# Optimization experiments

Hardware: AMD Instinct MI355X
Metric: run time of the kernel (lower is better)

## Reference

```python
import jax, jax.numpy as jnp
import numpy as np

EPS = 1e-5

def _bn(x, g, b, m, v):
    return (x - m) * jax.lax.rsqrt(v + EPS) * g + b

def setup_inputs() -> dict:
    key = jax.random.key(0)
    ks = jax.random.split(key, 40)
    B, D, H, O = 4096, 1723 * 6, 1024, 24 * 9 + 10
    d = {"x": jax.random.normal(ks[0], (B, D), jnp.float32)}
    def lin(i, din, dout):
        return (jax.random.normal(ks[i], (din, dout), jnp.float32) * (1.0 / np.sqrt(din)),
                jax.random.normal(ks[i + 1], (dout,), jnp.float32) * 0.01)
    def bnp(i, dout):
        return (jax.random.normal(ks[i], (dout,), jnp.float32) * 0.1 + 1.0,
                jax.random.normal(ks[i + 1], (dout,), jnp.float32) * 0.1,
                jax.random.normal(ks[i + 2], (dout,), jnp.float32) * 0.1,
                jax.random.uniform(ks[i + 3], (dout,), jnp.float32, 0.5, 1.5))
    d["W1"], d["b1"] = lin(1, D, H); d["g1"], d["be1"], d["m1"], d["v1"] = bnp(3, H)
    d["Wa"], d["ba"] = lin(7, H, H); d["ga"], d["bea"], d["ma"], d["va"] = bnp(9, H)
    d["Wb"], d["bb"] = lin(13, H, H); d["gb"], d["beb"], d["mb"], d["vb"] = bnp(15, H)
    d["Wc"], d["bc"] = lin(19, H, H); d["gc"], d["bec"], d["mc"], d["vc"] = bnp(21, H)
    d["Wd"], d["bd"] = lin(25, H, H); d["gd"], d["bed"], d["md"], d["vd"] = bnp(27, H)
    d["Wf"], d["bf"] = lin(31, H, O)
    return d

def reference(x, W1, b1, g1, be1, m1, v1,
              Wa, ba, ga, bea, ma, va,
              Wb, bb, gb, beb, mb, vb,
              Wc, bc, gc, bec, mc, vc,
              Wd, bd, gd, bed, md, vd,
              Wf, bf):
    B = x.shape[0]
    # FCBlock: Linear -> BN -> ReLU
    h = jax.nn.relu(_bn(x @ W1 + b1, g1, be1, m1, v1))
    # FCResBlock 1: relu(h + BN(Linear(relu(BN(Linear(h))))))
    t = jax.nn.relu(_bn(h @ Wa + ba, ga, bea, ma, va))
    t = _bn(t @ Wb + bb, gb, beb, mb, vb)
    h = jax.nn.relu(h + t)
    # FCResBlock 2
    t = jax.nn.relu(_bn(h @ Wc + bc, gc, bec, mc, vc))
    t = _bn(t @ Wd + bd, gd, bed, md, vd)
    h = jax.nn.relu(h + t)
    out = h @ Wf + bf  # [B, 226]
    rot = out[:, :216].reshape(-1, 3, 3)  # [B*24, 3, 3]
    betas = out[:, 216:]                   # [B, 10]
    U, S, Vh = jnp.linalg.svd(rot)         # batched 3x3 SVD
    R = jnp.matmul(U, Vh)                  # U V^T, closest orthogonal matrix
    det = jax.lax.stop_gradient(jnp.linalg.det(R))[:, None, None]  # torch computes det under no_grad
    R = (R * det).reshape(B, 24, 3, 3)
    return (R, betas)
```

## Files before the change

### kernel.cpp

```cpp
#include <hip/hip_runtime.h>
#include <hip/hip_bf16.h>

typedef unsigned int u32;
typedef unsigned short u16;
typedef _Float16 f16;
typedef __attribute__((ext_vector_type(8))) f16 f16x8;
typedef __attribute__((ext_vector_type(4))) float f32x4;
typedef __attribute__((ext_vector_type(4))) u16 u16x4;

#define NB 4096
#define DIN 10338
#define DPAD 10368
#define KC 5184
#define HD 1024
#define OD 226
#define OPAD 256
#define BN_EPS 1e-5f
#define RSC 0.00048828125f

__device__ __forceinline__ u16 f2h(float v) {
  f16 h = (f16)v;
  u16 r;
  __builtin_memcpy(&r, &h, 2);
  return r;
}
__device__ __forceinline__ void split2(float a, u16& s0, u16& s1) {
  f16 h0 = (f16)a;
  float r = (a - (float)h0) * 2048.0f;
  __builtin_memcpy(&s0, &h0, 2);
  s1 = f2h(r);
}

__device__ __forceinline__ void gload_lds16(const u16* g, u16* l) {
  __builtin_amdgcn_global_load_lds(
      (const __attribute__((address_space(1))) u32*)g,
      (__attribute__((address_space(3))) u32*)l, 16, 0, 0);
}

__global__ __launch_bounds__(256) void k_split_x(const float* __restrict__ x,
                                                 f16* __restrict__ p0,
                                                 f16* __restrict__ p1) {
  u32 idx = (blockIdx.x * 256u + threadIdx.x) * 4u;
  u32 row = idx / DPAD;
  u32 col = idx - row * DPAD;
  const float* s = x + (size_t)row * DIN + col;
  float v[4];
#pragma unroll
  for (int i = 0; i < 4; i++) {
    v[i] = ((int)col + i < DIN) ? s[i] : 0.f;
  }
  u16x4 o0, o1;
#pragma unroll
  for (int i = 0; i < 4; i++) {
    u16 a0, a1;
    split2(v[i], a0, a1);
    o0[i] = a0;
    o1[i] = a1;
  }
  *(u16x4*)((u16*)p0 + idx) = o0;
  *(u16x4*)((u16*)p1 + idx) = o1;
}

__global__ __launch_bounds__(256) void k_split_w(const float* __restrict__ W,
                                                 f16* __restrict__ p0,
                                                 f16* __restrict__ p1, int K,
                                                 int N, int Kp) {
  __shared__ float tile[32][33];
  int k0 = blockIdx.x * 32, n0 = blockIdx.y * 32;
  int tx = threadIdx.x, ty = threadIdx.y;
#pragma unroll
  for (int i = 0; i < 4; i++) {
    int k = k0 + ty + i * 8, n = n0 + tx;
    tile[ty + i * 8][tx] = (k < K && n < N) ? W[(size_t)k * N + n] : 0.f;
  }
  __syncthreads();
#pragma unroll
  for (int i = 0; i < 4; i++) {
    int n = n0 + ty + i * 8, k = k0 + tx;
    u16 s0, s1;
    split2(tile[tx][ty + i * 8], s0, s1);
    size_t o = (size_t)n * Kp + k;
    ((u16*)p0)[o] = s0;
    ((u16*)p1)[o] = s1;
  }
}

__global__ __launch_bounds__(512, 2) void k_gemm_big(
    const f16* __restrict__ A0p, const f16* __restrict__ A1p,
    const f16* __restrict__ B0p, const f16* __restrict__ B1p,
    float* __restrict__ P, int ldA, int ldB, int nk) {
  __shared__ __align__(16) u16 lds[3 * 24576];

  const u32 gx = gridDim.x, gy = gridDim.y;
  const u32 nwg = gx * gy * gridDim.z;
  u32 lin = blockIdx.x + gx * (blockIdx.y + gy * blockIdx.z);
  {
    const u32 q = nwg >> 3, r = nwg & 7;
    const u32 xcd = lin & 7, o = lin >> 3;
    lin = (xcd < r ? xcd * (q + 1) : r * (q + 1) + (xcd - r) * q) + o;
  }
  const u32 bz = lin / (gx * gy);
  const u32 rem = lin - bz * gx * gy;
  const u32 by = rem / gx;
  const u32 bx = rem - by * gx;
  const int m0 = by * 256, n0 = bx * 128;
  const size_t kbase = (size_t)bz * KC;

  const u16* __restrict__ A0u = (const u16*)A0p + kbase;
  const u16* __restrict__ A1u = (const u16*)A1p + kbase;
  const u16* __restrict__ B0u = (const u16*)B0p + kbase;
  const u16* __restrict__ B1u = (const u16*)B1p + kbase;
  float* __restrict__ Pz = P + (size_t)bz * NB * HD;

  const int t = threadIdx.x;
  const int lane = t & 63;
  const int wid = t >> 6;
  const int wm = wid >> 1, wn = wid & 1;
  const int l15 = lane & 15, l4 = lane >> 4;

  const int sgc = (((t & 3) ^ ((t >> 3) & 3)) << 3);
  const size_t gA0 = (size_t)(m0 + (t >> 2)) * ldA + sgc;
  const size_t gA1 = gA0 + (size_t)128 * ldA;
  const size_t gB = (size_t)(n0 + (t >> 2)) * ldB + sgc;
  const int dA0 = t * 8, dB = t * 8;

  int offA[4], offB[4];
#pragma unroll
  for (int mi = 0; mi < 4; mi++) {
    int row = wm * 64 + mi * 16 + l15;
    offA[mi] = row * 32 + ((l4 ^ ((row >> 1) & 3)) << 3);
  }
#pragma unroll
  for (int ni = 0; ni < 4; ni++) {
    int row = wn * 64 + ni * 16 + l15;
    offB[ni] = row * 32 + ((l4 ^ ((row >> 1) & 3)) << 3);
  }

  f32x4 hi[4][4], lo[4][4];
#pragma unroll
  for (int i = 0; i < 4; i++)
#pragma unroll
    for (int j = 0; j < 4; j++) {
      f32x4 z = {0.f, 0.f, 0.f, 0.f};
      hi[i][j] = z;
      lo[i][j] = z;
    }

#define STAGE_A0(Sb, ko)                         \
  gload_lds16(A0u + gA0 + (ko), (Sb) + dA0);     \
  gload_lds16(A0u + gA1 + (ko), (Sb) + 4096 + dA0);
#define STAGE_A1(Sb, ko)                              \
  gload_lds16(A1u + gA0 + (ko), (Sb) + 8192 + dA0);   \
  gload_lds16(A1u + gA1 + (ko), (Sb) + 12288 + dA0);
#define STAGE_B(Sb, ko)                               \
  gload_lds16(B0u + gB + (ko), (Sb) + 16384 + dB);    \
  gload_lds16(B1u + gB + (ko), (Sb) + 20480 + dB);

#define MFMA16(dst, af, bf)                                              \
  _Pragma("unroll") for (int mi = 0; mi < 4; mi++)                       \
      _Pragma("unroll") for (int ni = 0; ni < 4; ni++)                   \
          dst[mi][ni] = __builtin_amdgcn_mfma_f32_16x16x32_f16(          \
              af[mi], bf[ni], dst[mi][ni], 0, 0, 0);

  {
    u16* Sb0 = lds;
    u16* Sb1 = lds + 24576;
    STAGE_A0(Sb0, 0) STAGE_A1(Sb0, 0) STAGE_B(Sb0, 0)
    STAGE_A0(Sb1, 32) STAGE_A1(Sb1, 32) STAGE_B(Sb1, 32)
  }
  asm volatile("s_waitcnt vmcnt(6)" ::: "memory");
  __builtin_amdgcn_s_barrier();
  __builtin_amdgcn_sched_barrier(0);

  for (int tau = 0; tau < nk - 2; ++tau) {
    const u16* Lb = lds + (tau % 3) * 24576;
    u16* Sb = lds + ((tau + 2) % 3) * 24576;
    const size_t ko = (size_t)(tau + 2) * 32;
    f16x8 a0[4], b0[4], xf[4];

#pragma unroll
    for (int mi = 0; mi < 4; mi++) a0[mi] = *(const f16x8*)(Lb + offA[mi]);
#pragma unroll
    for (int ni = 0; ni < 4; ni++)
      b0[ni] = *(const f16x8*)(Lb + 16384 + offB[ni]);
    STAGE_A0(Sb, ko)
    __builtin_amdgcn_s_barrier();
    asm volatile("s_waitcnt lgkmcnt(0)" ::: "memory");
    __builtin_amdgcn_sched_barrier(0);
    __builtin_amdgcn_s_setprio(1);
    MFMA16(hi, a0, b0)
    __builtin_amdgcn_s_setprio(0);
    __builtin_amdgcn_s_barrier();

#pragma unroll
    for (int ni = 0; ni < 4; ni++)
      xf[ni] = *(const f16x8*)(Lb + 20480 + offB[ni]);
    STAGE_A1(Sb, ko)
    __builtin_amdgcn_s_barrier();
    asm volatile("s_waitcnt lgkmcnt(0)" ::: "memory");
    __builtin_amdgcn_sched_barrier(0);
    __builtin_amdgcn_s_setprio(1);
    MFMA16(lo, a0, xf)
    __builtin_amdgcn_s_setprio(0);
    __builtin_amdgcn_s_barrier();

#pragma unroll
    for (int mi = 0; mi < 4; mi++)
      xf[mi] = *(const f16x8*)(Lb + 8192 + offA[mi]);
    STAGE_B(Sb, ko)
    asm volatile("s_waitcnt vmcnt(6)" ::: "memory");
    __builtin_amdgcn_s_barrier();
    asm volatile("s_waitcnt lgkmcnt(0)" ::: "memory");
    __builtin_amdgcn_sched_barrier(0);
    __builtin_amdgcn_s_setprio(1);
    MFMA16(lo, xf, b0)
    __builtin_amdgcn_s_setprio(0);
    __builtin_amdgcn_s_barrier();
  }
  asm volatile("s_waitcnt vmcnt(0)" ::: "memory");
  __builtin_amdgcn_s_barrier();
  __builtin_amdgcn_sched_barrier(0);
#pragma unroll 1
  for (int tau = nk - 2; tau < nk; ++tau) {
    const u16* Lb = lds + (tau % 3) * 24576;
    f16x8 a0[4], b0[4], xf[4];
#pragma unroll
    for (int mi = 0; mi < 4; mi++) a0[mi] = *(const f16x8*)(Lb + offA[mi]);
#pragma unroll
    for (int ni = 0; ni < 4; ni++)
      b0[ni] = *(const f16x8*)(Lb + 16384 + offB[ni]);
    MFMA16(hi, a0, b0)
#pragma unroll
    for (int ni = 0; ni < 4; ni++)
      xf[ni] = *(const f16x8*)(Lb + 20480 + offB[ni]);
    MFMA16(lo, a0, xf)
#pragma unroll
    for (int mi = 0; mi < 4; mi++)
      xf[mi] = *(const f16x8*)(Lb + 8192 + offA[mi]);
    MFMA16(lo, xf, b0)
  }
#undef STAGE_A0
#undef STAGE_A1
#undef STAGE_B
#undef MFMA16

  const int rowb = m0 + wm * 64 + l4 * 4;
  const int colb = n0 + wn * 64 + l15;
#pragma unroll
  for (int mi = 0; mi < 4; mi++) {
#pragma unroll
    for (int ni = 0; ni < 4; ni++) {
      const int col = colb + ni * 16;
#pragma unroll
      for (int r = 0; r < 4; r++) {
        const int row = rowb + mi * 16 + r;
        Pz[(size_t)row * HD + col] = hi[mi][ni][r] + lo[mi][ni][r] * RSC;
      }
    }
  }
}

__global__ __launch_bounds__(256) void k_epi1(
    const float* __restrict__ P0, const float* __restrict__ P1,
    const float* __restrict__ bias, const float* __restrict__ gam,
    const float* __restrict__ bet, const float* __restrict__ mu,
    const float* __restrict__ var, float* __restrict__ hF,
    f16* __restrict__ h0, f16* __restrict__ h1) {
  const u32 i4 = (blockIdx.x * 256u + threadIdx.x) * 4u;
  const u32 col0 = i4 & (HD - 1);
  f32x4 a = *(const f32x4*)(P0 + i4);
  f32x4 b = *(const f32x4*)(P1 + i4);
  f32x4 y;
  u16x4 o0, o1;
#pragma unroll
  for (int e = 0; e < 4; e++) {
    const u32 c = col0 + e;
    float sc = gam[c] * rsqrtf(var[c] + BN_EPS);
    float v = ((a[e] + b[e]) + bias[c] - mu[c]) * sc + bet[c];
    v = fmaxf(v, 0.f);
    y[e] = v;
    u16 s0, s1;
    split2(v, s0, s1);
    o0[e] = s0;
    o1[e] = s1;
  }
  *(f32x4*)(hF + i4) = y;
  *(u16x4*)((u16*)h0 + i4) = o0;
  *(u16x4*)((u16*)h1 + i4) = o1;
}

template <int EPI>
__global__ __launch_bounds__(512, 2) void k_gemm_f(
    const f16* __restrict__ A0p, const f16* __restrict__ A1p,
    const f16* __restrict__ B0p, const f16* __restrict__ B1p,
    const float* __restrict__ bias, const float* __restrict__ gam,
    const float* __restrict__ bet, const float* __restrict__ mu,
    const float* __restrict__ var, const float* __restrict__ resF,
    float* __restrict__ hFout, f16* __restrict__ pl0, f16* __restrict__ pl1,
    float* __restrict__ oF, int ldA, int ldB, int nk, int ldout) {
  __shared__ __align__(16) u16 lds[4 * 16384];

  const u32 gx = gridDim.x, gy = gridDim.y;
  const u32 nwg = gx * gy;
  u32 lin = blockIdx.x + gx * blockIdx.y;
  {
    const u32 q = nwg >> 3, r = nwg & 7;
    const u32 xcd = lin & 7, o = lin >> 3;
    lin = (xcd < r ? xcd * (q + 1) : r * (q + 1) + (xcd - r) * q) + o;
  }
  const u32 by = lin / gx;
  const u32 bx = lin - by * gx;
  const int m0 = by * 128, n0 = bx * 128;

  const u16* __restrict__ A0u = (const u16*)A0p;
  const u16* __restrict__ A1u = (const u16*)A1p;
  const u16* __restrict__ B0u = (const u16*)B0p;
  const u16* __restrict__ B1u = (const u16*)B1p;

  const int t = threadIdx.x;
  const int lane = t & 63;
  const int wid = t >> 6;
  const int wm = wid >> 1, wn = wid & 1;
  const int l15 = lane & 15, l4 = lane >> 4;

  const int srow = t >> 2, sj = t & 3;
  const int sgc = ((sj ^ ((srow >> 1) & 3)) << 3);
  const size_t gA = (size_t)(m0 + srow) * ldA + sgc;
  const size_t gB = (size_t)(n0 + srow) * ldB + sgc;
  const int d0 = t * 8;

  int offA[2], offB[4];
#pragma unroll
  for (int mi = 0; mi < 2; mi++) {
    int row = wm * 32 + mi * 16 + l15;
    offA[mi] = row * 32 + ((l4 ^ ((row >> 1) & 3)) << 3);
  }
#pragma unroll
  for (int ni = 0; ni < 4; ni++) {
    int row = wn * 64 + ni * 16 + l15;
    offB[ni] = row * 32 + ((l4 ^ ((row >> 1) & 3)) << 3);
  }

  f32x4 hi[2][4], lo[2][4];
#pragma unroll
  for (int i = 0; i < 2; i++)
#pragma unroll
    for (int j = 0; j < 4; j++) {
      f32x4 z = {0.f, 0.f, 0.f, 0.f};
      hi[i][j] = z;
      lo[i][j] = z;
    }

#define STG_A0(Sb, ko) gload_lds16(A0u + gA + (ko), (Sb) + d0);
#define STG_A1(Sb, ko) gload_lds16(A1u + gA + (ko), (Sb) + 4096 + d0);
#define STG_B(Sb, ko)                               \
  gload_lds16(B0u + gB + (ko), (Sb) + 8192 + d0);   \
  gload_lds16(B1u + gB + (ko), (Sb) + 12288 + d0);
#define MFMA8(dst, af, bf)                                               \
  _Pragma("unroll") for (int mi = 0; mi < 2; mi++)                       \
      _Pragma("unroll") for (int ni = 0; ni < 4; ni++)                   \
          dst[mi][ni] = __builtin_amdgcn_mfma_f32_16x16x32_f16(          \
              af[mi], bf[ni], dst[mi][ni], 0, 0, 0);

  {
    u16* S0 = lds;
    u16* S1 = lds + 16384;
    u16* S2 = lds + 32768;
    STG_A0(S0, 0) STG_A1(S0, 0) STG_B(S0, 0)
    STG_A0(S1, 32) STG_A1(S1, 32) STG_B(S1, 32)
    STG_A0(S2, 64) STG_A1(S2, 64) STG_B(S2, 64)
  }
  asm volatile("s_waitcnt vmcnt(8)" ::: "memory");
  __builtin_amdgcn_s_barrier();
  __builtin_amdgcn_sched_barrier(0);

  for (int tau = 0; tau < nk - 3; ++tau) {
    const u16* Lb = lds + (tau & 3) * 16384;
    u16* Sb = lds + ((tau + 3) & 3) * 16384;
    const size_t ko = (size_t)(tau + 3) * 32;
    f16x8 a0[2], b0[4], xf[4];

#pragma unroll
    for (int mi = 0; mi < 2; mi++) a0[mi] = *(const f16x8*)(Lb + offA[mi]);
#pragma unroll
    for (int ni = 0; ni < 4; ni++)
      b0[ni] = *(const f16x8*)(Lb + 8192 + offB[ni]);
    STG_A0(Sb, ko)
    __builtin_amdgcn_s_barrier();
    asm volatile("s_waitcnt lgkmcnt(0)" ::: "memory");
    __builtin_amdgcn_sched_barrier(0);
    __builtin_amdgcn_s_setprio(1);
    MFMA8(hi, a0, b0)
    __builtin_amdgcn_s_setprio(0);
    __builtin_amdgcn_s_barrier();

#pragma unroll
    for (int ni = 0; ni < 4; ni++)
      xf[ni] = *(const f16x8*)(Lb + 12288 + offB[ni]);
    STG_A1(Sb, ko)
    __builtin_amdgcn_s_barrier();
    asm volatile("s_waitcnt lgkmcnt(0)" ::: "memory");
    __builtin_amdgcn_sched_barrier(0);
    __builtin_amdgcn_s_setprio(1);
    MFMA8(lo, a0, xf)
    __builtin_amdgcn_s_setprio(0);
    __builtin_amdgcn_s_barrier();

#pragma unroll
    for (int mi = 0; mi < 2; mi++)
      xf[mi] = *(const f16x8*)(Lb + 4096 + offA[mi]);
    STG_B(Sb, ko)
    asm volatile("s_waitcnt vmcnt(8)" ::: "memory");
    __builtin_amdgcn_s_barrier();
    asm volatile("s_waitcnt lgkmcnt(0)" ::: "memory");
    __builtin_amdgcn_sched_barrier(0);
    __builtin_amdgcn_s_setprio(1);
    MFMA8(lo, xf, b0)
    __builtin_amdgcn_s_setprio(0);
    __builtin_amdgcn_s_barrier();
  }
  asm volatile("s_waitcnt vmcnt(0)" ::: "memory");
  __builtin_amdgcn_s_barrier();
  __builtin_amdgcn_sched_barrier(0);
#pragma unroll 1
  for (int tau = nk - 3; tau < nk; ++tau) {
    const u16* Lb = lds + (tau & 3) * 16384;
    f16x8 a0[2], b0[4], xf[4];
#pragma unroll
    for (int mi = 0; mi < 2; mi++) a0[mi] = *(const f16x8*)(Lb + offA[mi]);
#pragma unroll
    for (int ni = 0; ni < 4; ni++)
      b0[ni] = *(const f16x8*)(Lb + 8192 + offB[ni]);
    MFMA8(hi, a0, b0)
#pragma unroll
    for (int ni = 0; ni < 4; ni++)
      xf[ni] = *(const f16x8*)(Lb + 12288 + offB[ni]);
    MFMA8(lo, a0, xf)
#pragma unroll
    for (int mi = 0; mi < 2; mi++)
      xf[mi] = *(const f16x8*)(Lb + 4096 + offA[mi]);
    MFMA8(lo, xf, b0)
  }
#undef STG_A0
#undef STG_A1
#undef STG_B
#undef MFMA8

  const int rowb = m0 + wm * 32 + l4 * 4;
  const int colb = n0 + wn * 64 + l15;
#pragma unroll
  for (int ni = 0; ni < 4; ni++) {
    const int col = colb + ni * 16;
    float sc = 1.f, pb = 0.f;
    if (EPI == 4) {
      pb = (col < OD) ? bias[col] : 0.f;
    } else {
      sc = gam[col] * rsqrtf(var[col] + BN_EPS);
      pb = (bias[col] - mu[col]) * sc + bet[col];
    }
#pragma unroll
    for (int mi = 0; mi < 2; mi++) {
#pragma unroll
      for (int r = 0; r < 4; r++) {
        const int row = rowb + mi * 16 + r;
        float s = hi[mi][ni][r] + lo[mi][ni][r] * RSC;
        if (EPI == 4) {
          oF[(size_t)row * ldout + col] = s + pb;
          continue;
        }
        float v = s * sc + pb;
        if (EPI == 2 || EPI == 3) v += resF[(size_t)row * HD + col];
        v = fmaxf(v, 0.f);
        if (EPI == 2) hFout[(size_t)row * HD + col] = v;
        u16 s0, s1;
        split2(v, s0, s1);
        size_t o = (size_t)row * HD + col;
        ((u16*)pl0)[o] = s0;
        ((u16*)pl1)[o] = s1;
      }
    }
  }
}

__global__ __launch_bounds__(256) void k_polar(const float* __restrict__ oF,
                                               float* __restrict__ R) {
  int g = blockIdx.x * 256 + threadIdx.x;
  if (g >= NB * 24) return;
  int b = g / 24, j = g - b * 24;
  const float* p = oF + (size_t)b * OPAD + j * 9;
  float xv[9];
#pragma unroll
  for (int e = 0; e < 9; e++) xv[e] = p[e];
#pragma unroll 1
  for (int it = 0; it < 18; it++) {
    float c0 = xv[4] * xv[8] - xv[5] * xv[7];
    float c1 = xv[5] * xv[6] - xv[3] * xv[8];
    float c2 = xv[3] * xv[7] - xv[4] * xv[6];
    float c3 = xv[2] * xv[7] - xv[1] * xv[8];
    float c4 = xv[0] * xv[8] - xv[2] * xv[6];
    float c5 = xv[1] * xv[6] - xv[0] * xv[7];
    float c6 = xv[1] * xv[5] - xv[2] * xv[4];
    float c7 = xv[2] * xv[3] - xv[0] * xv[5];
    float c8 = xv[0] * xv[4] - xv[1] * xv[3];
    float det = xv[0] * c0 + xv[1] * c1 + xv[2] * c2;
    if (fabsf(det) < 1e-30f) break;
    float inv = 1.f / det;
    float y0 = c0 * inv, y1 = c1 * inv, y2 = c2 * inv;
    float y3 = c3 * inv, y4 = c4 * inv, y5 = c5 * inv;
    float y6 = c6 * inv, y7 = c7 * inv, y8 = c8 * inv;
    float gmm = 1.f;
    if (it < 8) {
      float nx = xv[0]*xv[0]+xv[1]*xv[1]+xv[2]*xv[2]+xv[3]*xv[3]+xv[4]*xv[4]
               + xv[5]*xv[5]+xv[6]*xv[6]+xv[7]*xv[7]+xv[8]*xv[8];
      float ny = y0*y0+y1*y1+y2*y2+y3*y3+y4*y4+y5*y5+y6*y6+y7*y7+y8*y8;
      gmm = sqrtf(sqrtf(ny / nx));
    }
    float a0 = 0.5f * gmm, a1 = 0.5f / gmm;
    xv[0] = a0 * xv[0] + a1 * y0; xv[1] = a0 * xv[1] + a1 * y1;
    xv[2] = a0 * xv[2] + a1 * y2; xv[3] = a0 * xv[3] + a1 * y3;
    xv[4] = a0 * xv[4] + a1 * y4; xv[5] = a0 * xv[5] + a1 * y5;
    xv[6] = a0 * xv[6] + a1 * y6; xv[7] = a0 * xv[7] + a1 * y7;
    xv[8] = a0 * xv[8] + a1 * y8;
  }
  float dfin = xv[0] * (xv[4] * xv[8] - xv[5] * xv[7])
             + xv[1] * (xv[5] * xv[6] - xv[3] * xv[8])
             + xv[2] * (xv[3] * xv[7] - xv[4] * xv[6]);
  float s = (dfin > 0.f) ? 1.f : -1.f;
  float* q = R + (size_t)g * 9;
#pragma unroll
  for (int e = 0; e < 9; e++) q[e] = s * xv[e];
}

__global__ __launch_bounds__(256) void k_betas(const float* __restrict__ oF,
                                               float* __restrict__ dst) {
  int i = blockIdx.x * 256 + threadIdx.x;
  if (i >= NB * 10) return;
  int b = i / 10, j = i - b * 10;
  dst[i] = oF[(size_t)b * OPAD + 216 + j];
}

extern "C" void kernel_launch(void* const* d_in, const int* in_sizes, int n_in,
                              void* d_out, int out_size, void* d_ws, size_t ws_size,
                              hipStream_t stream) {
  const float* x   = (const float*)d_in[0];
  const float* W1  = (const float*)d_in[1];
  const float* b1  = (const float*)d_in[2];
  const float* g1  = (const float*)d_in[3];
  const float* be1 = (const float*)d_in[4];
  const float* m1  = (const float*)d_in[5];
  const float* v1  = (const float*)d_in[6];
  const float* Wa  = (const float*)d_in[7];
  const float* ba  = (const float*)d_in[8];
  const float* ga  = (const float*)d_in[9];
  const float* bea = (const float*)d_in[10];
  const float* ma  = (const float*)d_in[11];
  const float* va  = (const float*)d_in[12];
  const float* Wb  = (const float*)d_in[13];
  const float* bb  = (const float*)d_in[14];
  const float* gb  = (const float*)d_in[15];
  const float* beb = (const float*)d_in[16];
  const float* mb  = (const float*)d_in[17];
  const float* vb  = (const float*)d_in[18];
  const float* Wc  = (const float*)d_in[19];
  const float* bc  = (const float*)d_in[20];
  const float* gc  = (const float*)d_in[21];
  const float* bec = (const float*)d_in[22];
  const float* mc  = (const float*)d_in[23];
  const float* vc  = (const float*)d_in[24];
  const float* Wd  = (const float*)d_in[25];
  const float* bd  = (const float*)d_in[26];
  const float* gd  = (const float*)d_in[27];
  const float* bed = (const float*)d_in[28];
  const float* md  = (const float*)d_in[29];
  const float* vd  = (const float*)d_in[30];
  const float* Wf  = (const float*)d_in[31];
  const float* bf  = (const float*)d_in[32];
  (void)in_sizes; (void)n_in; (void)out_size; (void)ws_size;

  char* ws = (char*)d_ws;
  size_t off = 0;
  auto alloc = [&](size_t bytes) -> void* {
    void* p = ws + off;
    off += (bytes + 255) & ~(size_t)255;
    return p;
  };
  f16* xp0 = (f16*)alloc((size_t)NB * DPAD * 2);
  f16* xp1 = (f16*)alloc((size_t)NB * DPAD * 2);
  f16* w1p0 = (f16*)alloc((size_t)HD * DPAD * 2);
  f16* w1p1 = (f16*)alloc((size_t)HD * DPAD * 2);
  f16* wap0 = (f16*)alloc((size_t)HD * HD * 2);
  f16* wap1 = (f16*)alloc((size_t)HD * HD * 2);
  f16* wbp0 = (f16*)alloc((size_t)HD * HD * 2);
  f16* wbp1 = (f16*)alloc((size_t)HD * HD * 2);
  f16* wcp0 = (f16*)alloc((size_t)HD * HD * 2);
  f16* wcp1 = (f16*)alloc((size_t)HD * HD * 2);
  f16* wdp0 = (f16*)alloc((size_t)HD * HD * 2);
  f16* wdp1 = (f16*)alloc((size_t)HD * HD * 2);
  f16* wfp0 = (f16*)alloc((size_t)OPAD * HD * 2);
  f16* wfp1 = (f16*)alloc((size_t)OPAD * HD * 2);
  float* P = (float*)alloc((size_t)2 * NB * HD * 4);
  f16* h0 = (f16*)xp0;
  f16* h1 = h0 + (size_t)NB * HD;
  f16* t0 = h1 + (size_t)NB * HD;
  f16* t1 = t0 + (size_t)NB * HD;
  float* hF = (float*)(t1 + (size_t)NB * HD);
  float* oF = hF + (size_t)NB * HD;

  k_split_x<<<NB * DPAD / 4 / 256, 256, 0, stream>>>(x, xp0, xp1);
  dim3 tb(32, 8);
  k_split_w<<<dim3(DPAD / 32, HD / 32), tb, 0, stream>>>(W1, w1p0, w1p1, DIN, HD, DPAD);
  k_split_w<<<dim3(HD / 32, HD / 32), tb, 0, stream>>>(Wa, wap0, wap1, HD, HD, HD);
  k_split_w<<<dim3(HD / 32, HD / 32), tb, 0, stream>>>(Wb, wbp0, wbp1, HD, HD, HD);
  k_split_w<<<dim3(HD / 32, HD / 32), tb, 0, stream>>>(Wc, wcp0, wcp1, HD, HD, HD);
  k_split_w<<<dim3(HD / 32, HD / 32), tb, 0, stream>>>(Wd, wdp0, wdp1, HD, HD, HD);
  k_split_w<<<dim3(HD / 32, OPAD / 32), tb, 0, stream>>>(Wf, wfp0, wfp1, HD, OD, HD);

  dim3 g1g(HD / 128, NB / 256, 2);
  dim3 gg(HD / 128, NB / 128);
  dim3 gf(OPAD / 128, NB / 128);

  k_gemm_big<<<g1g, 512, 0, stream>>>(xp0, xp1, w1p0, w1p1, P, DPAD, DPAD,
                                      KC / 32);
  k_epi1<<<NB * HD / 4 / 256, 256, 0, stream>>>(P, P + (size_t)NB * HD, b1, g1,
                                                be1, m1, v1, hF, h0, h1);
  k_gemm_f<1><<<gg, 512, 0, stream>>>(
      h0, h1, wap0, wap1, ba, ga, bea, ma, va, nullptr, nullptr, t0, t1,
      nullptr, HD, HD, HD / 32, HD);
  k_gemm_f<2><<<gg, 512, 0, stream>>>(
      t0, t1, wbp0, wbp1, bb, gb, beb, mb, vb, hF, hF, h0, h1, nullptr, HD,
      HD, HD / 32, HD);
  k_gemm_f<1><<<gg, 512, 0, stream>>>(
      h0, h1, wcp0, wcp1, bc, gc, bec, mc, vc, nullptr, nullptr, t0, t1,
      nullptr, HD, HD, HD / 32, HD);
  k_gemm_f<3><<<gg, 512, 0, stream>>>(
      t0, t1, wdp0, wdp1, bd, gd, bed, md, vd, hF, nullptr, h0, h1, nullptr,
      HD, HD, HD / 32, HD);
  k_gemm_f<4><<<gf, 512, 0, stream>>>(
      h0, h1, wfp0, wfp1, bf, nullptr, nullptr, nullptr, nullptr, nullptr,
      nullptr, nullptr, nullptr, oF, HD, HD, HD / 32, OPAD);

  float* Rout = (float*)d_out;
  k_polar<<<(NB * 24 + 255) / 256, 256, 0, stream>>>(oF, Rout);
  k_betas<<<(NB * 10 + 255) / 256, 256, 0, stream>>>(oF, Rout + (size_t)NB * 216);
}
```

Measured before the change: 523.6 us.

## Restructure split-f16 GEMM main loops to one barrier per k-step with prefetched fragments

Both GEMM kernels now issue all global-to-LDS stages for a future k-tile at the start of each iteration. The per-iteration barriers drop from six to one, and the s_waitcnt/sched_barrier fences between the three MFMA groups are removed. The next tile's A0 fragments are prefetched from LDS during the last MFMA group, and the separate epilogue loops are folded into the main loop with guards and partial unrolling. The aim is to cut barrier and wait stalls so LDS reads overlap MFMA work. The trade-off is higher register pressure, and LDS buffer reuse now depends on a single barrier per iteration being enough.

```diff
diff --git a/kernel.cpp b/kernel.cpp
--- a/kernel.cpp
+++ b/kernel.cpp
@@ -146,15 +146,15 @@
       lo[i][j] = z;
     }
 
-#define STAGE_A0(Sb, ko)                         \
-  gload_lds16(A0u + gA0 + (ko), (Sb) + dA0);     \
-  gload_lds16(A0u + gA1 + (ko), (Sb) + 4096 + dA0);
-#define STAGE_A1(Sb, ko)                              \
-  gload_lds16(A1u + gA0 + (ko), (Sb) + 8192 + dA0);   \
-  gload_lds16(A1u + gA1 + (ko), (Sb) + 12288 + dA0);
-#define STAGE_B(Sb, ko)                               \
-  gload_lds16(B0u + gB + (ko), (Sb) + 16384 + dB);    \
-  gload_lds16(B1u + gB + (ko), (Sb) + 20480 + dB);
+#define STAGEB(Sb, ko)                                   \
+  {                                                      \
+    gload_lds16(A0u + gA0 + (ko), (Sb) + dA0);           \
+    gload_lds16(A0u + gA1 + (ko), (Sb) + 4096 + dA0);    \
+    gload_lds16(A1u + gA0 + (ko), (Sb) + 8192 + dA0);    \
+    gload_lds16(A1u + gA1 + (ko), (Sb) + 12288 + dA0);   \
+    gload_lds16(B0u + gB + (ko), (Sb) + 16384 + dB);     \
+    gload_lds16(B1u + gB + (ko), (Sb) + 20480 + dB);     \
+  }
 
 #define MFMA16(dst, af, bf)                                              \
   _Pragma("unroll") for (int mi = 0; mi < 4; mi++)                       \
@@ -162,86 +162,57 @@
           dst[mi][ni] = __builtin_amdgcn_mfma_f32_16x16x32_f16(          \
               af[mi], bf[ni], dst[mi][ni], 0, 0, 0);
 
-  {
-    u16* Sb0 = lds;
-    u16* Sb1 = lds + 24576;
-    STAGE_A0(Sb0, 0) STAGE_A1(Sb0, 0) STAGE_B(Sb0, 0)
-    STAGE_A0(Sb1, 32) STAGE_A1(Sb1, 32) STAGE_B(Sb1, 32)
-  }
+  STAGEB(lds, 0)
+  STAGEB(lds + 24576, 32)
   asm volatile("s_waitcnt vmcnt(6)" ::: "memory");
   __builtin_amdgcn_s_barrier();
-  __builtin_amdgcn_sched_barrier(0);
-
-  for (int tau = 0; tau < nk - 2; ++tau) {
+
+  f16x8 a0[4];
+#pragma unroll
+  for (int mi = 0; mi < 4; mi++) a0[mi] = *(const f16x8*)(lds + offA[mi]);
+
+#pragma unroll 3
+  for (int tau = 0; tau < nk; ++tau) {
     const u16* Lb = lds + (tau % 3) * 24576;
     u16* Sb = lds + ((tau + 2) % 3) * 24576;
     const size_t ko = (size_t)(tau + 2) * 32;
-    f16x8 a0[4], b0[4], xf[4];
-
-#pragma unroll
-    for (int mi = 0; mi < 4; mi++) a0[mi] = *(const f16x8*)(Lb + offA[mi]);
+    if (tau + 2 < nk) STAGEB(Sb, ko)
+
+    f16x8 b0[4], b1[4], a1[4], a0n[4];
 #pragma unroll
     for (int ni = 0; ni < 4; ni++)
       b0[ni] = *(const f16x8*)(Lb + 16384 + offB[ni]);
-    STAGE_A0(Sb, ko)
-    __builtin_amdgcn_s_barrier();
-    asm volatile("s_waitcnt lgkmcnt(0)" ::: "memory");
-    __builtin_amdgcn_sched_barrier(0);
     __builtin_amdgcn_s_setprio(1);
     MFMA16(hi, a0, b0)
     __builtin_amdgcn_s_setprio(0);
+
+#pragma unroll
+    for (int ni = 0; ni < 4; ni++)
+      b1[ni] = *(const f16x8*)(Lb + 20480 + offB[ni]);
+    __builtin_amdgcn_s_setprio(1);
+    MFMA16(lo, a0, b1)
+    __builtin_amdgcn_s_setprio(0);
+
+#pragma unroll
+    for (int mi = 0; mi < 4; mi++)
+      a1[mi] = *(const f16x8*)(Lb + 8192 + offA[mi]);
+    if (tau + 1 < nk) {
+      const u16* Ln = lds + ((tau + 1) % 3) * 24576;
+      asm volatile("s_waitcnt vmcnt(6)" ::: "memory");
+#pragma unroll
+      for (int mi = 0; mi < 4; mi++)
+        a0n[mi] = *(const f16x8*)(Ln + offA[mi]);
+    }
+    __builtin_amdgcn_s_setprio(1);
+    MFMA16(lo, a1, b0)
+    __builtin_amdgcn_s_setprio(0);
+    if (tau + 1 < nk) {
+#pragma unroll
+      for (int mi = 0; mi < 4; mi++) a0[mi] = a0n[mi];
+    }
     __builtin_amdgcn_s_barrier();
-
-#pragma unroll
-    for (int ni = 0; ni < 4; ni++)
-      xf[ni] = *(const f16x8*)(Lb + 20480 + offB[ni]);
-    STAGE_A1(Sb, ko)
-    __builtin_amdgcn_s_barrier();
-    asm volatile("s_waitcnt lgkmcnt(0)" ::: "memory");
-    __builtin_amdgcn_sched_barrier(0);
-    __builtin_amdgcn_s_setprio(1);
-    MFMA16(lo, a0, xf)
-    __builtin_amdgcn_s_setprio(0);
-    __builtin_amdgcn_s_barrier();
-
-#pragma unroll
-    for (int mi = 0; mi < 4; mi++)
-      xf[mi] = *(const f16x8*)(Lb + 8192 + offA[mi]);
-    STAGE_B(Sb, ko)
-    asm volatile("s_waitcnt vmcnt(6)" ::: "memory");
-    __builtin_amdgcn_s_barrier();
-    asm volatile("s_waitcnt lgkmcnt(0)" ::: "memory");
-    __builtin_amdgcn_sched_barrier(0);
-    __builtin_amdgcn_s_setprio(1);
-    MFMA16(lo, xf, b0)
-    __builtin_amdgcn_s_setprio(0);
-    __builtin_amdgcn_s_barrier();
-  }
-  asm volatile("s_waitcnt vmcnt(0)" ::: "memory");
-  __builtin_amdgcn_s_barrier();
-  __builtin_amdgcn_sched_barrier(0);
-#pragma unroll 1
-  for (int tau = nk - 2; tau < nk; ++tau) {
-    const u16* Lb = lds + (tau % 3) * 24576;
-    f16x8 a0[4], b0[4], xf[4];
-#pragma unroll
-    for (int mi = 0; mi < 4; mi++) a0[mi] = *(const f16x8*)(Lb + offA[mi]);
-#pragma unroll
-    for (int ni = 0; ni < 4; ni++)
-      b0[ni] = *(const f16x8*)(Lb + 16384 + offB[ni]);
-    MFMA16(hi, a0, b0)
-#pragma unroll
-    for (int ni = 0; ni < 4; ni++)
-      xf[ni] = *(const f16x8*)(Lb + 20480 + offB[ni]);
-    MFMA16(lo, a0, xf)
-#pragma unroll
-    for (int mi = 0; mi < 4; mi++)
-      xf[mi] = *(const f16x8*)(Lb + 8192 + offA[mi]);
-    MFMA16(lo, xf, b0)
-  }
-#undef STAGE_A0
-#undef STAGE_A1
-#undef STAGE_B
+  }
+#undef STAGEB
 #undef MFMA16
 
   const int rowb = m0 + wm * 64 + l4 * 4;
@@ -351,99 +322,71 @@
       lo[i][j] = z;
     }
 
-#define STG_A0(Sb, ko) gload_lds16(A0u + gA + (ko), (Sb) + d0);
-#define STG_A1(Sb, ko) gload_lds16(A1u + gA + (ko), (Sb) + 4096 + d0);
-#define STG_B(Sb, ko)                               \
-  gload_lds16(B0u + gB + (ko), (Sb) + 8192 + d0);   \
-  gload_lds16(B1u + gB + (ko), (Sb) + 12288 + d0);
+#define STAGE(Sb, ko)                                 \
+  {                                                   \
+    gload_lds16(A0u + gA + (ko), (Sb) + d0);          \
+    gload_lds16(A1u + gA + (ko), (Sb) + 4096 + d0);   \
+    gload_lds16(B0u + gB + (ko), (Sb) + 8192 + d0);   \
+    gload_lds16(B1u + gB + (ko), (Sb) + 12288 + d0);  \
+  }
 #define MFMA8(dst, af, bf)                                               \
   _Pragma("unroll") for (int mi = 0; mi < 2; mi++)                       \
       _Pragma("unroll") for (int ni = 0; ni < 4; ni++)                   \
           dst[mi][ni] = __builtin_amdgcn_mfma_f32_16x16x32_f16(          \
               af[mi], bf[ni], dst[mi][ni], 0, 0, 0);
 
-  {
-    u16* S0 = lds;
-    u16* S1 = lds + 16384;
-    u16* S2 = lds + 32768;
-    STG_A0(S0, 0) STG_A1(S0, 0) STG_B(S0, 0)
-    STG_A0(S1, 32) STG_A1(S1, 32) STG_B(S1, 32)
-    STG_A0(S2, 64) STG_A1(S2, 64) STG_B(S2, 64)
-  }
+  STAGE(lds, 0)
+  STAGE(lds + 16384, 32)
+  STAGE(lds + 32768, 64)
   asm volatile("s_waitcnt vmcnt(8)" ::: "memory");
   __builtin_amdgcn_s_barrier();
-  __builtin_amdgcn_sched_barrier(0);
-
-  for (int tau = 0; tau < nk - 3; ++tau) {
+
+  f16x8 a0[2];
+#pragma unroll
+  for (int mi = 0; mi < 2; mi++) a0[mi] = *(const f16x8*)(lds + offA[mi]);
+
+#pragma unroll 4
+  for (int tau = 0; tau < nk; ++tau) {
     const u16* Lb = lds + (tau & 3) * 16384;
     u16* Sb = lds + ((tau + 3) & 3) * 16384;
     const size_t ko = (size_t)(tau + 3) * 32;
-    f16x8 a0[2], b0[4], xf[4];
-
-#pragma unroll
-    for (int mi = 0; mi < 2; mi++) a0[mi] = *(const f16x8*)(Lb + offA[mi]);
+    if (tau + 3 < nk) STAGE(Sb, ko)
+
+    f16x8 b0[4], b1[4], a1[2], a0n[2];
 #pragma unroll
     for (int ni = 0; ni < 4; ni++)
       b0[ni] = *(const f16x8*)(Lb + 8192 + offB[ni]);
-    STG_A0(Sb, ko)
-    __builtin_amdgcn_s_barrier();
-    asm volatile("s_waitcnt lgkmcnt(0)" ::: "memory");
-    __builtin_amdgcn_sched_barrier(0);
     __builtin_amdgcn_s_setprio(1);
     MFMA8(hi, a0, b0)
     __builtin_amdgcn_s_setprio(0);
+
+#pragma unroll
+    for (int ni = 0; ni < 4; ni++)
+      b1[ni] = *(const f16x8*)(Lb + 12288 + offB[ni]);
+    __builtin_amdgcn_s_setprio(1);
+    MFMA8(lo, a0, b1)
+    __builtin_amdgcn_s_setprio(0);
+
+#pragma unroll
+    for (int mi = 0; mi < 2; mi++)
+      a1[mi] = *(const f16x8*)(Lb + 4096 + offA[mi]);
+    if (tau + 1 < nk) {
+      const u16* Ln = lds + ((tau + 1) & 3) * 16384;
+      asm volatile("s_waitcnt vmcnt(8)" ::: "memory");
+#pragma unroll
+      for (int mi = 0; mi < 2; mi++)
+        a0n[mi] = *(const f16x8*)(Ln + offA[mi]);
+    }
+    __builtin_amdgcn_s_setprio(1);
+    MFMA8(lo, a1, b0)
+    __builtin_amdgcn_s_setprio(0);
+    if (tau + 1 < nk) {
+#pragma unroll
+      for (int mi = 0; mi < 2; mi++) a0[mi] = a0n[mi];
+    }
     __builtin_amdgcn_s_barrier();
-
-#pragma unroll
-    for (int ni = 0; ni < 4; ni++)
-      xf[ni] = *(const f16x8*)(Lb + 12288 + offB[ni]);
-    STG_A1(Sb, ko)
-    __builtin_amdgcn_s_barrier();
-    asm volatile("s_waitcnt lgkmcnt(0)" ::: "memory");
-    __builtin_amdgcn_sched_barrier(0);
-    __builtin_amdgcn_s_setprio(1);
-    MFMA8(lo, a0, xf)
-    __builtin_amdgcn_s_setprio(0);
-    __builtin_amdgcn_s_barrier();
-
-#pragma unroll
-    for (int mi = 0; mi < 2; mi++)
-      xf[mi] = *(const f16x8*)(Lb + 4096 + offA[mi]);
-    STG_B(Sb, ko)
-    asm volatile("s_waitcnt vmcnt(8)" ::: "memory");
-    __builtin_amdgcn_s_barrier();
-    asm volatile("s_waitcnt lgkmcnt(0)" ::: "memory");
-    __builtin_amdgcn_sched_barrier(0);
-    __builtin_amdgcn_s_setprio(1);
-    MFMA8(lo, xf, b0)
-    __builtin_amdgcn_s_setprio(0);
-    __builtin_amdgcn_s_barrier();
-  }
-  asm volatile("s_waitcnt vmcnt(0)" ::: "memory");
-  __builtin_amdgcn_s_barrier();
-  __builtin_amdgcn_sched_barrier(0);
-#pragma unroll 1
-  for (int tau = nk - 3; tau < nk; ++tau) {
-    const u16* Lb = lds + (tau & 3) * 16384;
-    f16x8 a0[2], b0[4], xf[4];
-#pragma unroll
-    for (int mi = 0; mi < 2; mi++) a0[mi] = *(const f16x8*)(Lb + offA[mi]);
-#pragma unroll
-    for (int ni = 0; ni < 4; ni++)
-      b0[ni] = *(const f16x8*)(Lb + 8192 + offB[ni]);
-    MFMA8(hi, a0, b0)
-#pragma unroll
-    for (int ni = 0; ni < 4; ni++)
-      xf[ni] = *(const f16x8*)(Lb + 12288 + offB[ni]);
-    MFMA8(lo, a0, xf)
-#pragma unroll
-    for (int mi = 0; mi < 2; mi++)
-      xf[mi] = *(const f16x8*)(Lb + 4096 + offA[mi]);
-    MFMA8(lo, xf, b0)
-  }
-#undef STG_A0
-#undef STG_A1
-#undef STG_B
+  }
+#undef STAGE
 #undef MFMA8
 
   const int rowb = m0 + wm * 32 + l4 * 4;
```

After: 546.1 us. 1.04x slower.

## Fuse fp32 input split into first GEMM and batch hidden weight splits

Applied to the files above, without the earlier changes.

Removes the separate pass that converts x into two fp16 planes. The big GEMM now reads fp32 x directly into registers, splits each value into hi and lo halves, and writes them into the swizzled LDS tiles, while B still arrives by direct global-to-LDS loads. This avoids writing and re-reading about 170 MB of intermediate planes, at the cost of more register pressure, a full vmcnt(0) wait each iteration, and split arithmetic inside the GEMM loop. The four hidden-weight split launches are also merged into one launch using a z-indexed pointer pack.

```diff
diff --git a/kernel.cpp b/kernel.cpp
--- a/kernel.cpp
+++ b/kernel.cpp
@@ -5,6 +5,7 @@
 typedef unsigned short u16;
 typedef _Float16 f16;
 typedef __attribute__((ext_vector_type(8))) f16 f16x8;
+typedef __attribute__((ext_vector_type(8))) u16 u16x8;
 typedef __attribute__((ext_vector_type(4))) float f32x4;
 typedef __attribute__((ext_vector_type(4))) u16 u16x4;
 
@@ -37,30 +38,6 @@
       (__attribute__((address_space(3))) u32*)l, 16, 0, 0);
 }
 
-__global__ __launch_bounds__(256) void k_split_x(const float* __restrict__ x,
-                                                 f16* __restrict__ p0,
-                                                 f16* __restrict__ p1) {
-  u32 idx = (blockIdx.x * 256u + threadIdx.x) * 4u;
-  u32 row = idx / DPAD;
-  u32 col = idx - row * DPAD;
-  const float* s = x + (size_t)row * DIN + col;
-  float v[4];
-#pragma unroll
-  for (int i = 0; i < 4; i++) {
-    v[i] = ((int)col + i < DIN) ? s[i] : 0.f;
-  }
-  u16x4 o0, o1;
-#pragma unroll
-  for (int i = 0; i < 4; i++) {
-    u16 a0, a1;
-    split2(v[i], a0, a1);
-    o0[i] = a0;
-    o1[i] = a1;
-  }
-  *(u16x4*)((u16*)p0 + idx) = o0;
-  *(u16x4*)((u16*)p1 + idx) = o1;
-}
-
 __global__ __launch_bounds__(256) void k_split_w(const float* __restrict__ W,
                                                  f16* __restrict__ p0,
                                                  f16* __restrict__ p1, int K,
@@ -85,10 +62,38 @@
   }
 }
 
+struct WPack {
+  const float* W[4];
+  f16* p0[4];
+  f16* p1[4];
+};
+__global__ __launch_bounds__(256) void k_split_w4(WPack wp) {
+  __shared__ float tile[32][33];
+  const float* __restrict__ W = wp.W[blockIdx.z];
+  f16* __restrict__ p0 = wp.p0[blockIdx.z];
+  f16* __restrict__ p1 = wp.p1[blockIdx.z];
+  int k0 = blockIdx.x * 32, n0 = blockIdx.y * 32;
+  int tx = threadIdx.x, ty = threadIdx.y;
+#pragma unroll
+  for (int i = 0; i < 4; i++) {
+    int k = k0 + ty + i * 8, n = n0 + tx;
+    tile[ty + i * 8][tx] = W[(size_t)k * HD + n];
+  }
+  __syncthreads();
+#pragma unroll
+  for (int i = 0; i < 4; i++) {
+    int n = n0 + ty + i * 8, k = k0 + tx;
+    u16 s0, s1;
+    split2(tile[tx][ty + i * 8], s0, s1);
+    size_t o = (size_t)n * HD + k;
+    ((u16*)p0)[o] = s0;
+    ((u16*)p1)[o] = s1;
+  }
+}
+
 __global__ __launch_bounds__(512, 2) void k_gemm_big(
-    const f16* __restrict__ A0p, const f16* __restrict__ A1p,
-    const f16* __restrict__ B0p, const f16* __restrict__ B1p,
-    float* __restrict__ P, int ldA, int ldB, int nk) {
+    const float* __restrict__ X, const f16* __restrict__ B0p,
+    const f16* __restrict__ B1p, float* __restrict__ P, int ldB, int nk) {
   __shared__ __align__(16) u16 lds[3 * 24576];
 
   const u32 gx = gridDim.x, gy = gridDim.y;
@@ -104,10 +109,8 @@
   const u32 by = rem / gx;
   const u32 bx = rem - by * gx;
   const int m0 = by * 256, n0 = bx * 128;
-  const size_t kbase = (size_t)bz * KC;
-
-  const u16* __restrict__ A0u = (const u16*)A0p + kbase;
-  const u16* __restrict__ A1u = (const u16*)A1p + kbase;
+  const int kbase = (int)bz * KC;
+
   const u16* __restrict__ B0u = (const u16*)B0p + kbase;
   const u16* __restrict__ B1u = (const u16*)B1p + kbase;
   float* __restrict__ Pz = P + (size_t)bz * NB * HD;
@@ -119,10 +122,15 @@
   const int l15 = lane & 15, l4 = lane >> 4;
 
   const int sgc = (((t & 3) ^ ((t >> 3) & 3)) << 3);
-  const size_t gA0 = (size_t)(m0 + (t >> 2)) * ldA + sgc;
-  const size_t gA1 = gA0 + (size_t)128 * ldA;
   const size_t gB = (size_t)(n0 + (t >> 2)) * ldB + sgc;
-  const int dA0 = t * 8, dB = t * 8;
+  const int dB = t * 8;
+
+  const int arow = t >> 1;
+  const int acol = (t & 1) * 16;
+  const float* __restrict__ xrow = X + (size_t)(m0 + arow) * DIN;
+  const int swzA = (arow >> 1) & 3;
+  const int wofA0 = arow * 32 + ((((acol >> 3) + 0) ^ swzA) << 3);
+  const int wofA1 = arow * 32 + ((((acol >> 3) + 1) ^ swzA) << 3);
 
   int offA[4], offB[4];
 #pragma unroll
@@ -146,12 +154,46 @@
       lo[i][j] = z;
     }
 
-#define STAGE_A0(Sb, ko)                         \
-  gload_lds16(A0u + gA0 + (ko), (Sb) + dA0);     \
-  gload_lds16(A0u + gA1 + (ko), (Sb) + 4096 + dA0);
-#define STAGE_A1(Sb, ko)                              \
-  gload_lds16(A1u + gA0 + (ko), (Sb) + 8192 + dA0);   \
-  gload_lds16(A1u + gA1 + (ko), (Sb) + 12288 + dA0);
+  float2 av[8];
+
+#define AREG_LOAD(klocal)                                            \
+  {                                                                  \
+    const int cg = kbase + (klocal) + acol;                          \
+    if (cg + 16 <= DIN) {                                            \
+      _Pragma("unroll") for (int j = 0; j < 8; j++)                  \
+          av[j] = *(const float2*)(xrow + cg + 2 * j);               \
+    } else {                                                         \
+      _Pragma("unroll") for (int j = 0; j < 8; j++) {                \
+        const int c = cg + 2 * j;                                    \
+        av[j].x = (c < DIN) ? xrow[c] : 0.f;                         \
+        av[j].y = (c + 1 < DIN) ? xrow[c + 1] : 0.f;                 \
+      }                                                              \
+    }                                                                \
+  }
+
+#define ASPLIT_WRITE(Sb)                                             \
+  {                                                                  \
+    u16x8 q0a, q0b, q1a, q1b;                                        \
+    _Pragma("unroll") for (int j = 0; j < 4; j++) {                  \
+      u16 s0x, s1x, s0y, s1y;                                        \
+      split2(av[j].x, s0x, s1x);                                     \
+      split2(av[j].y, s0y, s1y);                                     \
+      q0a[2 * j] = s0x; q0a[2 * j + 1] = s0y;                        \
+      q1a[2 * j] = s1x; q1a[2 * j + 1] = s1y;                        \
+    }                                                                \
+    _Pragma("unroll") for (int j = 0; j < 4; j++) {                  \
+      u16 s0x, s1x, s0y, s1y;                                        \
+      split2(av[4 + j].x, s0x, s1x);                                 \
+      split2(av[4 + j].y, s0y, s1y);                                 \
+      q0b[2 * j] = s0x; q0b[2 * j + 1] = s0y;                        \
+      q1b[2 * j] = s1x; q1b[2 * j + 1] = s1y;                        \
+    }                                                                \
+    *(u16x8*)((Sb) + wofA0) = q0a;                                   \
+    *(u16x8*)((Sb) + wofA1) = q0b;                                   \
+    *(u16x8*)((Sb) + 8192 + wofA0) = q1a;                            \
+    *(u16x8*)((Sb) + 8192 + wofA1) = q1b;                            \
+  }
+
 #define STAGE_B(Sb, ko)                               \
   gload_lds16(B0u + gB + (ko), (Sb) + 16384 + dB);    \
   gload_lds16(B1u + gB + (ko), (Sb) + 20480 + dB);
@@ -162,28 +204,32 @@
           dst[mi][ni] = __builtin_amdgcn_mfma_f32_16x16x32_f16(          \
               af[mi], bf[ni], dst[mi][ni], 0, 0, 0);
 
-  {
-    u16* Sb0 = lds;
-    u16* Sb1 = lds + 24576;
-    STAGE_A0(Sb0, 0) STAGE_A1(Sb0, 0) STAGE_B(Sb0, 0)
-    STAGE_A0(Sb1, 32) STAGE_A1(Sb1, 32) STAGE_B(Sb1, 32)
-  }
-  asm volatile("s_waitcnt vmcnt(6)" ::: "memory");
+  STAGE_B(lds, 0)
+  STAGE_B(lds + 24576, 32)
+  AREG_LOAD(0)
+  asm volatile("s_waitcnt vmcnt(0)" ::: "memory");
+  ASPLIT_WRITE(lds)
+  AREG_LOAD(32)
+  asm volatile("s_waitcnt vmcnt(0)" ::: "memory");
+  ASPLIT_WRITE(lds + 24576)
+  asm volatile("s_waitcnt lgkmcnt(0)" ::: "memory");
   __builtin_amdgcn_s_barrier();
   __builtin_amdgcn_sched_barrier(0);
 
   for (int tau = 0; tau < nk - 2; ++tau) {
     const u16* Lb = lds + (tau % 3) * 24576;
     u16* Sb = lds + ((tau + 2) % 3) * 24576;
-    const size_t ko = (size_t)(tau + 2) * 32;
+    const int ko = (tau + 2) * 32;
     f16x8 a0[4], b0[4], xf[4];
 
+    STAGE_B(Sb, (size_t)ko)
+    AREG_LOAD(ko)
+
 #pragma unroll
     for (int mi = 0; mi < 4; mi++) a0[mi] = *(const f16x8*)(Lb + offA[mi]);
 #pragma unroll
     for (int ni = 0; ni < 4; ni++)
       b0[ni] = *(const f16x8*)(Lb + 16384 + offB[ni]);
-    STAGE_A0(Sb, ko)
     __builtin_amdgcn_s_barrier();
     asm volatile("s_waitcnt lgkmcnt(0)" ::: "memory");
     __builtin_amdgcn_sched_barrier(0);
@@ -195,7 +241,6 @@
 #pragma unroll
     for (int ni = 0; ni < 4; ni++)
       xf[ni] = *(const f16x8*)(Lb + 20480 + offB[ni]);
-    STAGE_A1(Sb, ko)
     __builtin_amdgcn_s_barrier();
     asm volatile("s_waitcnt lgkmcnt(0)" ::: "memory");
     __builtin_amdgcn_sched_barrier(0);
@@ -207,8 +252,8 @@
 #pragma unroll
     for (int mi = 0; mi < 4; mi++)
       xf[mi] = *(const f16x8*)(Lb + 8192 + offA[mi]);
-    STAGE_B(Sb, ko)
-    asm volatile("s_waitcnt vmcnt(6)" ::: "memory");
+    asm volatile("s_waitcnt vmcnt(0)" ::: "memory");
+    ASPLIT_WRITE(Sb)
     __builtin_amdgcn_s_barrier();
     asm volatile("s_waitcnt lgkmcnt(0)" ::: "memory");
     __builtin_amdgcn_sched_barrier(0);
@@ -217,7 +262,7 @@
     __builtin_amdgcn_s_setprio(0);
     __builtin_amdgcn_s_barrier();
   }
-  asm volatile("s_waitcnt vmcnt(0)" ::: "memory");
+  asm volatile("s_waitcnt lgkmcnt(0)" ::: "memory");
   __builtin_amdgcn_s_barrier();
   __builtin_amdgcn_sched_barrier(0);
 #pragma unroll 1
@@ -239,8 +284,8 @@
       xf[mi] = *(const f16x8*)(Lb + 8192 + offA[mi]);
     MFMA16(lo, xf, b0)
   }
-#undef STAGE_A0
-#undef STAGE_A1
+#undef AREG_LOAD
+#undef ASPLIT_WRITE
 #undef STAGE_B
 #undef MFMA16
 
@@ -584,8 +629,6 @@
     off += (bytes + 255) & ~(size_t)255;
     return p;
   };
-  f16* xp0 = (f16*)alloc((size_t)NB * DPAD * 2);
-  f16* xp1 = (f16*)alloc((size_t)NB * DPAD * 2);
   f16* w1p0 = (f16*)alloc((size_t)HD * DPAD * 2);
   f16* w1p1 = (f16*)alloc((size_t)HD * DPAD * 2);
   f16* wap0 = (f16*)alloc((size_t)HD * HD * 2);
@@ -599,28 +642,27 @@
   f16* wfp0 = (f16*)alloc((size_t)OPAD * HD * 2);
   f16* wfp1 = (f16*)alloc((size_t)OPAD * HD * 2);
   float* P = (float*)alloc((size_t)2 * NB * HD * 4);
-  f16* h0 = (f16*)xp0;
-  f16* h1 = h0 + (size_t)NB * HD;
-  f16* t0 = h1 + (size_t)NB * HD;
-  f16* t1 = t0 + (size_t)NB * HD;
-  float* hF = (float*)(t1 + (size_t)NB * HD);
-  float* oF = hF + (size_t)NB * HD;
-
-  k_split_x<<<NB * DPAD / 4 / 256, 256, 0, stream>>>(x, xp0, xp1);
+  f16* h0 = (f16*)alloc((size_t)NB * HD * 2);
+  f16* h1 = (f16*)alloc((size_t)NB * HD * 2);
+  f16* t0 = (f16*)alloc((size_t)NB * HD * 2);
+  f16* t1 = (f16*)alloc((size_t)NB * HD * 2);
+  float* hF = (float*)alloc((size_t)NB * HD * 4);
+  float* oF = (float*)alloc((size_t)NB * OPAD * 4);
+
   dim3 tb(32, 8);
   k_split_w<<<dim3(DPAD / 32, HD / 32), tb, 0, stream>>>(W1, w1p0, w1p1, DIN, HD, DPAD);
-  k_split_w<<<dim3(HD / 32, HD / 32), tb, 0, stream>>>(Wa, wap0, wap1, HD, HD, HD);
-  k_split_w<<<dim3(HD / 32, HD / 32), tb, 0, stream>>>(Wb, wbp0, wbp1, HD, HD, HD);
-  k_split_w<<<dim3(HD / 32, HD / 32), tb, 0, stream>>>(Wc, wcp0, wcp1, HD, HD, HD);
-  k_split_w<<<dim3(HD / 32, HD / 32), tb, 0, stream>>>(Wd, wdp0, wdp1, HD, HD, HD);
+  WPack wp;
+  wp.W[0] = Wa; wp.W[1] = Wb; wp.W[2] = Wc; wp.W[3] = Wd;
+  wp.p0[0] = wap0; wp.p0[1] = wbp0; wp.p0[2] = wcp0; wp.p0[3] = wdp0;
+  wp.p1[0] = wap1; wp.p1[1] = wbp1; wp.p1[2] = wcp1; wp.p1[3] = wdp1;
+  k_split_w4<<<dim3(HD / 32, HD / 32, 4), tb, 0, stream>>>(wp);
   k_split_w<<<dim3(HD / 32, OPAD / 32), tb, 0, stream>>>(Wf, wfp0, wfp1, HD, OD, HD);
 
   dim3 g1g(HD / 128, NB / 256, 2);
   dim3 gg(HD / 128, NB / 128);
   dim3 gf(OPAD / 128, NB / 128);
 
-  k_gemm_big<<<g1g, 512, 0, stream>>>(xp0, xp1, w1p0, w1p1, P, DPAD, DPAD,
-                                      KC / 32);
+  k_gemm_big<<<g1g, 512, 0, stream>>>(x, w1p0, w1p1, P, DPAD, KC / 32);
   k_epi1<<<NB * HD / 4 / 256, 256, 0, stream>>>(P, P + (size_t)NB * HD, b1, g1,
                                                 be1, m1, v1, hF, h0, h1);
   k_gemm_f<1><<<gg, 512, 0, stream>>>(
```

Result: slower. 570.9 us (+9.0%).
